# Kernel tuning notes

Hardware: AMD Instinct MI355X
Metric: run time of the kernel (lower is better)

The kernel has to match this reference:

```python
import jax, jax.numpy as jnp
import numpy as np

DN = ('NDHWC', 'DHWIO', 'NDHWC')
EPS = 1e-5  # torch BatchNorm default

def _conv(x, w, s):
    # Minkowski conv, kernel 3 centered: output coord j gathers input coords s*j + {-1,0,1}
    return jax.lax.conv_general_dilated(x, w, (s, s, s), ((1, 1),) * 3, dimension_numbers=DN)

def _convt(x, w):
    # stride-2 transpose conv, kernel 3 centered: output p gets input c where 2c in {p-1,p,p+1}
    return jax.lax.conv_general_dilated(x, w, (1, 1, 1), ((1, 2),) * 3,
                                        lhs_dilation=(2, 2, 2), dimension_numbers=DN)

def _down(m):
    # stride-2 coordinate map: a coarse voxel is active iff any of its 2x2x2 fine voxels is
    B, G = m.shape[0], m.shape[1]
    return m.reshape(B, G // 2, 2, G // 2, 2, G // 2, 2).any(axis=(2, 4, 6))

def _mbn(h, m, g, b):
    # MinkowskiBatchNorm: BatchNorm1d over the active (sparse) feature rows only
    mf = m[..., None].astype(h.dtype)
    h = h * mf
    cnt = jnp.maximum(jnp.sum(mf), 1.0)
    mean = jnp.sum(h, axis=(0, 1, 2, 3)) / cnt
    var = jnp.sum(((h - mean) * mf) ** 2, axis=(0, 1, 2, 3)) / cnt
    return ((h - mean) * jax.lax.rsqrt(var + EPS) * g + b) * mf


def setup_inputs() -> dict:
    key = jax.random.key(0)
    ks = jax.random.split(key, 8)
    B, G, Cin, Cout = 2, 64, 4, 16
    def w(k, shape, fan):
        return jax.random.normal(k, shape, jnp.float32) * np.float32(1.0 / np.sqrt(fan))
    return {
        'x': jax.random.normal(ks[0], (B, G, G, G, Cin), jnp.float32),
        'mask': jax.random.bernoulli(ks[1], 0.1, (B, G, G, G)),
        'w1': w(ks[2], (3, 3, 3, Cin, 8), 27 * Cin), 'g1': jnp.ones(8), 'b1': jnp.zeros(8),
        'w2': w(ks[3], (3, 3, 3, 8, 16), 27 * 8), 'g2': jnp.ones(16), 'b2': jnp.zeros(16),
        'w3': w(ks[4], (3, 3, 3, 16, 32), 27 * 16), 'g3': jnp.ones(32), 'b3': jnp.zeros(32),
        'w3t': w(ks[5], (3, 3, 3, 32, 16), 27 * 32), 'g3t': jnp.ones(16), 'b3t': jnp.zeros(16),
        'w2t': w(ks[6], (3, 3, 3, 32, 16), 27 * 32), 'g2t': jnp.ones(16), 'b2t': jnp.zeros(16),
        'w1x1': w(ks[7], (24, Cout), 24),
    }


def reference(x, mask, w1, g1, b1, w2, g2, b2, w3, g3, b3,
              w3t, g3t, b3t, w2t, g2t, b2t, w1x1):
    m1 = mask
    m2 = _down(m1)
    m4 = _down(m2)
    mf1 = m1[..., None].astype(x.dtype)

    xs = x * mf1                                      # sparse tensor: zero at inactive coords
    s1 = _mbn(_conv(xs, w1, 1), m1, g1, b1)           # block1, stride 1
    o = jax.nn.relu(s1)
    s2 = _mbn(_conv(o, w2, 2), m2, g2, b2)            # block2, stride 2
    o = jax.nn.relu(s2)
    s4 = _mbn(_conv(o, w3, 2), m4, g3, b3)            # block3, stride 4
    o = jax.nn.relu(s4)

    o = jax.nn.relu(_mbn(_convt(o, w3t), m2, g3t, b3t))   # block3_tr -> stride-2 coords
    o = jnp.concatenate([o, s2], axis=-1)                 # ME.cat(out, out_s2) -> 32 ch
    o = jax.nn.relu(_mbn(_convt(o, w2t), m1, g2t, b2t))   # block2_tr -> stride-1 coords
    o = jnp.concatenate([o, s1], axis=-1)                 # ME.cat(out, out_s1) -> 24 ch
    return jnp.einsum('bdhwc,co->bdhwo', o, w1x1) * mf1   # conv1_tr: 1x1x1 conv
```

## Files before the change

kernel.cpp:

```cpp
#include <hip/hip_runtime.h>

#define NVOX1 524288
#define NVOX2 65536
#define NVOX4 8192

#define ST_SUM1 16
#define ST_SQ1  24
#define ST_SUM2 32
#define ST_SQ2  48
#define ST_SUM3 64
#define ST_SQ3  96
#define ST_SUM3T 128
#define ST_SQ3T  144
#define ST_SUM2T 160
#define ST_SQ2T  176
#define FLAG_OFF 200
#define IC_N1 204
#define IC_N2 205
#define IC_N4 206
#define ST_ZERO 256

#define OFF_M1C 512
#define OFF_M2  (OFF_M1C + NVOX1)
#define OFF_M4  (OFF_M2 + NVOX2)
#define OFF_H1  (OFF_M4 + NVOX4)
#define OFF_S2  (OFF_H1 + NVOX1 * 8)
#define OFF_H3  (OFF_S2 + NVOX2 * 16)
#define OFF_T3  (OFF_H3 + NVOX4 * 32)
#define OFF_L1  (OFF_T3 + NVOX2 * 16)
#define OFF_L2  (OFF_L1 + NVOX1)
#define OFF_L4  (OFF_L2 + NVOX2)
#define OFF_BC1 (OFF_L4 + NVOX4)
#define OFF_BC2 (OFF_BC1 + 2048)
#define OFF_BC4 (OFF_BC2 + 256)

#define EPSBN 1e-5f

__device__ __forceinline__ void ttaps(int p, int gin, int* c, int* k, int* ok) {
  c[0] = p >> 1; k[0] = (p & 1) ? 0 : 1; ok[0] = 1;
  int cb = (p + 1) >> 1;
  int o = (p & 1) && (cb < gin);
  c[1] = o ? cb : 0; k[1] = 2; ok[1] = o;
}

__device__ __forceinline__ void stat_flush8(float* sum, float* sq, float* s_sum, float* s_sq, int t) {
#pragma unroll
  for (int off = 1; off < 64; off <<= 1)
#pragma unroll
    for (int c = 0; c < 8; c++) {
      sum[c] += __shfl_xor(sum[c], off, 64);
      sq[c]  += __shfl_xor(sq[c], off, 64);
    }
  if ((t & 63) == 0) {
#pragma unroll
    for (int c = 0; c < 8; c++) { atomicAdd(&s_sum[c], sum[c]); atomicAdd(&s_sq[c], sq[c]); }
  }
}

__global__ __launch_bounds__(256) void k_detect(const unsigned int* __restrict__ m,
                                                int* __restrict__ flags) {
  int tid = blockIdx.x * 256 + threadIdx.x;
  int hasf = 0, hasb = 0;
  for (int i = tid; i < NVOX1; i += 256 * 256) {
    unsigned int v = m[i];
    if (v == 0x3F800000u) hasf = 1;
    else if (v > 1u) hasb = 1;
  }
  hasf = __syncthreads_or(hasf);
  hasb = __syncthreads_or(hasb);
  if (threadIdx.x == 0) {
    if (hasf) atomicOr(&flags[0], 1);
    if (hasb) atomicOr(&flags[1], 1);
  }
}

__global__ __launch_bounds__(256) void k_canon(const void* __restrict__ mraw,
                                               int* __restrict__ m1c,
                                               const int* __restrict__ flags,
                                               int* __restrict__ blkcnt1) {
  int idx = blockIdx.x * 256 + threadIdx.x;
  int isf = flags[0], isb = flags[1];
  int v;
  if (isf)      v = (((const float*)mraw)[idx] != 0.f);
  else if (isb) v = (((const unsigned char*)mraw)[idx] != 0);
  else          v = (((const int*)mraw)[idx] != 0);
  m1c[idx] = v;
  int c = __syncthreads_count(v);
  if (threadIdx.x == 0) blkcnt1[blockIdx.x] = c;
}

__global__ __launch_bounds__(256) void k_down1(const int* __restrict__ m1,
                                               int* __restrict__ m2,
                                               int* __restrict__ blkcnt2) {
  int idx = blockIdx.x * 256 + threadIdx.x;
  int x = idx & 31, y = (idx >> 5) & 31, z = (idx >> 10) & 31, b = idx >> 15;
  int any = 0;
#pragma unroll
  for (int dz = 0; dz < 2; dz++)
#pragma unroll
    for (int dy = 0; dy < 2; dy++)
#pragma unroll
      for (int dx = 0; dx < 2; dx++)
        any |= m1[((b * 64 + 2 * z + dz) * 64 + 2 * y + dy) * 64 + 2 * x + dx];
  any = any ? 1 : 0;
  m2[idx] = any;
  int c = __syncthreads_count(any);
  if (threadIdx.x == 0) blkcnt2[blockIdx.x] = c;
}

__global__ __launch_bounds__(256) void k_down2(const int* __restrict__ m2,
                                               int* __restrict__ m4,
                                               int* __restrict__ blkcnt4) {
  int idx = blockIdx.x * 256 + threadIdx.x;
  int x = idx & 15, y = (idx >> 4) & 15, z = (idx >> 8) & 15, b = idx >> 12;
  int any = 0;
#pragma unroll
  for (int dz = 0; dz < 2; dz++)
#pragma unroll
    for (int dy = 0; dy < 2; dy++)
#pragma unroll
      for (int dx = 0; dx < 2; dx++)
        any |= m2[((b * 32 + 2 * z + dz) * 32 + 2 * y + dy) * 32 + 2 * x + dx];
  any = any ? 1 : 0;
  m4[idx] = any;
  int c = __syncthreads_count(any);
  if (threadIdx.x == 0) blkcnt4[blockIdx.x] = c;
}

__global__ __launch_bounds__(1024) void k_scan(int* __restrict__ bc1,
                                               int* __restrict__ bc2,
                                               int* __restrict__ bc4,
                                               int* __restrict__ cnts) {
  __shared__ int sA[2048], sB[2048];
  int* a; int n; int outIdx;
  if (blockIdx.x == 0)      { a = bc1; n = 2048; outIdx = IC_N1; }
  else if (blockIdx.x == 1) { a = bc2; n = 256;  outIdx = IC_N2; }
  else                      { a = bc4; n = 32;   outIdx = IC_N4; }
  int t = threadIdx.x;
  int i0 = t, i1 = t + 1024;
  int v0 = (i0 < n) ? a[i0] : 0;
  int v1 = (i1 < n) ? a[i1] : 0;
  sA[i0] = v0; sA[i1] = v1;
  __syncthreads();
  int* src = sA; int* dst = sB;
  for (int st = 1; st < 2048; st <<= 1) {
    int x0 = src[i0]; if (i0 >= st) x0 += src[i0 - st];
    int x1 = src[i1]; if (i1 >= st) x1 += src[i1 - st];
    dst[i0] = x0; dst[i1] = x1;
    __syncthreads();
    int* tmp = src; src = dst; dst = tmp;
  }
  if (i0 < n) a[i0] = src[i0] - v0;
  if (i1 < n) a[i1] = src[i1] - v1;
  if (t == 0) cnts[outIdx] = src[2047];
}

__global__ __launch_bounds__(256) void k_scatter(const int* __restrict__ m1,
                                                 const int* __restrict__ m2,
                                                 const int* __restrict__ m4,
                                                 const int* __restrict__ bc1,
                                                 const int* __restrict__ bc2,
                                                 const int* __restrict__ bc4,
                                                 int* __restrict__ list1,
                                                 int* __restrict__ list2,
                                                 int* __restrict__ list4) {
  __shared__ int s_w[4];
  int bid = blockIdx.x, t = threadIdx.x;
  const int* mask; const int* base; int* list; int lb;
  if (bid < 2048)      { mask = m1; base = bc1; list = list1; lb = bid; }
  else if (bid < 2304) { mask = m2; base = bc2; list = list2; lb = bid - 2048; }
  else                 { mask = m4; base = bc4; list = list4; lb = bid - 2304; }
  int idx = lb * 256 + t;
  int act = mask[idx];
  unsigned long long b = __ballot(act != 0);
  int lane = t & 63, wid = t >> 6;
  if (lane == 0) s_w[wid] = __popcll(b);
  __syncthreads();
  int wbase = 0;
  for (int i = 0; i < wid; i++) wbase += s_w[i];
  if (act) {
    int pre = __popcll(b & ((1ull << lane) - 1ull));
    list[base[lb] + wbase + pre] = idx;
  }
}

__global__ __launch_bounds__(256) void k_conv1(const float* __restrict__ x,
                                               const int* __restrict__ m1,
                                               const int* __restrict__ list1,
                                               const int* __restrict__ cnts,
                                               const float* __restrict__ w,
                                               float* __restrict__ h1,
                                               float* __restrict__ stats) {
  __shared__ float s_w[27 * 32];
  __shared__ float s_sum[8], s_sq[8];
  int t = threadIdx.x;
  { const float4* w4 = (const float4*)w; float4* sw4 = (float4*)s_w;
    for (int i = t; i < 216; i += 256) sw4[i] = w4[i]; }
  if (t < 8) { s_sum[t] = 0.f; s_sq[t] = 0.f; }
  __syncthreads();
  int n = cnts[IC_N1];
  float sum[8], sq[8];
#pragma unroll
  for (int c = 0; c < 8; c++) { sum[c] = 0.f; sq[c] = 0.f; }
  for (int i = blockIdx.x * 256 + t; i < n; i += gridDim.x * 256) {
    int v = list1[i];
    int vx = v & 63, vy = (v >> 6) & 63, vz = (v >> 12) & 63, vb = v >> 18;
    float acc[8];
#pragma unroll
    for (int c = 0; c < 8; c++) acc[c] = 0.f;
#pragma unroll
    for (int kd = 0; kd < 3; kd++) { int d = vz + kd - 1; if ((unsigned)d >= 64u) continue;
#pragma unroll
      for (int kh = 0; kh < 3; kh++) { int h = vy + kh - 1; if ((unsigned)h >= 64u) continue;
#pragma unroll
        for (int kw = 0; kw < 3; kw++) { int ww = vx + kw - 1; if ((unsigned)ww >= 64u) continue;
          int ni = ((vb * 64 + d) * 64 + h) * 64 + ww;
          if (!m1[ni]) continue;
          float4 ip = *(const float4*)(x + (size_t)ni * 4);
          const float* wp = s_w + ((kd * 3 + kh) * 3 + kw) * 32;
#pragma unroll
          for (int co = 0; co < 8; co++) {
            float a = fmaf(ip.x, wp[co], acc[co]);
            a = fmaf(ip.y, wp[8 + co], a);
            a = fmaf(ip.z, wp[16 + co], a);
            acc[co] = fmaf(ip.w, wp[24 + co], a);
          }
        } } }
    float4* hp = (float4*)(h1 + (size_t)v * 8);
    float4 q0 = {acc[0], acc[1], acc[2], acc[3]};
    float4 q1 = {acc[4], acc[5], acc[6], acc[7]};
    hp[0] = q0; hp[1] = q1;
#pragma unroll
    for (int c = 0; c < 8; c++) { sum[c] += acc[c]; sq[c] += acc[c] * acc[c]; }
  }
  stat_flush8(sum, sq, s_sum, s_sq, t);
  __syncthreads();
  if (t < 8) {
    if (s_sum[t] != 0.f) atomicAdd(&stats[ST_SUM1 + t], s_sum[t]);
    if (s_sq[t]  != 0.f) atomicAdd(&stats[ST_SQ1 + t], s_sq[t]);
  }
}

__global__ __launch_bounds__(256) void k_conv2(const float* __restrict__ h1,
                                               const int* __restrict__ m1,
                                               const int* __restrict__ list2,
                                               const int* __restrict__ cnts,
                                               const float* __restrict__ w,
                                               const float* __restrict__ g1,
                                               const float* __restrict__ b1,
                                               float* __restrict__ s2,
                                               float* __restrict__ stats) {
  __shared__ float s_w[27 * 8 * 8];
  __shared__ float s_sc[8], s_bi[8];
  __shared__ float s_sum[8], s_sq[8];
  int t = threadIdx.x, g = blockIdx.y;
  for (int i = t; i < 432; i += 256) {
    int r = i >> 1, half = i & 1;
    *(float4*)(s_w + r * 8 + half * 4) = *(const float4*)(w + r * 16 + g * 8 + half * 4);
  }
  if (t < 8) {
    float cnt = fmaxf((float)cnts[IC_N1], 1.f);
    float mean = stats[ST_SUM1 + t] / cnt;
    float var = fmaxf(stats[ST_SQ1 + t] / cnt - mean * mean, 0.f);
    float sc = g1[t] * rsqrtf(var + EPSBN);
    s_sc[t] = sc; s_bi[t] = b1[t] - mean * sc;
    s_sum[t] = 0.f; s_sq[t] = 0.f;
  }
  __syncthreads();
  int n = cnts[IC_N2];
  float sum[8], sq[8];
#pragma unroll
  for (int c = 0; c < 8; c++) { sum[c] = 0.f; sq[c] = 0.f; }
  for (int i = blockIdx.x * 256 + t; i < n; i += gridDim.x * 256) {
    int v = list2[i];
    int vx = v & 31, vy = (v >> 5) & 31, vz = (v >> 10) & 31, vb = v >> 15;
    float acc[8];
#pragma unroll
    for (int c = 0; c < 8; c++) acc[c] = 0.f;
#pragma unroll
    for (int kd = 0; kd < 3; kd++) { int d = 2 * vz + kd - 1; if (d < 0) continue;
#pragma unroll
      for (int kh = 0; kh < 3; kh++) { int h = 2 * vy + kh - 1; if (h < 0) continue;
#pragma unroll
        for (int kw = 0; kw < 3; kw++) { int ww = 2 * vx + kw - 1; if (ww < 0) continue;
          int ni = ((vb * 64 + d) * 64 + h) * 64 + ww;
          if (!m1[ni]) continue;
          float4 i0 = *(const float4*)(h1 + (size_t)ni * 8);
          float4 i1 = *(const float4*)(h1 + (size_t)ni * 8 + 4);
          float r[8] = {i0.x, i0.y, i0.z, i0.w, i1.x, i1.y, i1.z, i1.w};
          const float* wp = s_w + ((kd * 3 + kh) * 3 + kw) * 64;
#pragma unroll
          for (int ci = 0; ci < 8; ci++) {
            float vv = fmaxf(fmaf(r[ci], s_sc[ci], s_bi[ci]), 0.f);
#pragma unroll
            for (int co = 0; co < 8; co++) acc[co] = fmaf(vv, wp[ci * 8 + co], acc[co]);
          }
        } } }
    float4* sp = (float4*)(s2 + (size_t)v * 16 + g * 8);
    float4 q0 = {acc[0], acc[1], acc[2], acc[3]};
    float4 q1 = {acc[4], acc[5], acc[6], acc[7]};
    sp[0] = q0; sp[1] = q1;
#pragma unroll
    for (int c = 0; c < 8; c++) { sum[c] += acc[c]; sq[c] += acc[c] * acc[c]; }
  }
  stat_flush8(sum, sq, s_sum, s_sq, t);
  __syncthreads();
  if (t < 8) {
    if (s_sum[t] != 0.f) atomicAdd(&stats[ST_SUM2 + g * 8 + t], s_sum[t]);
    if (s_sq[t]  != 0.f) atomicAdd(&stats[ST_SQ2 + g * 8 + t], s_sq[t]);
  }
}

__global__ __launch_bounds__(256) void k_conv3(const float* __restrict__ s2raw,
                                               const int* __restrict__ m2,
                                               const int* __restrict__ list4,
                                               const int* __restrict__ cnts,
                                               const float* __restrict__ w,
                                               const float* __restrict__ g2,
                                               const float* __restrict__ b2,
                                               float* __restrict__ h3,
                                               float* __restrict__ stats) {
  __shared__ float s_w[27 * 16 * 8];
  __shared__ float s_sc[16], s_bi[16];
  __shared__ float s_sum[8], s_sq[8];
  int t = threadIdx.x, g = blockIdx.y;
  for (int i = t; i < 864; i += 256) {
    int r = i >> 1, half = i & 1;
    *(float4*)(s_w + r * 8 + half * 4) = *(const float4*)(w + r * 32 + g * 8 + half * 4);
  }
  if (t < 16) {
    float cnt = fmaxf((float)cnts[IC_N2], 1.f);
    float mean = stats[ST_SUM2 + t] / cnt;
    float var = fmaxf(stats[ST_SQ2 + t] / cnt - mean * mean, 0.f);
    float sc = g2[t] * rsqrtf(var + EPSBN);
    s_sc[t] = sc; s_bi[t] = b2[t] - mean * sc;
  }
  if (t < 8) { s_sum[t] = 0.f; s_sq[t] = 0.f; }
  __syncthreads();
  int n = cnts[IC_N4];
  float sum[8], sq[8];
#pragma unroll
  for (int c = 0; c < 8; c++) { sum[c] = 0.f; sq[c] = 0.f; }
  for (int i = blockIdx.x * 256 + t; i < n; i += gridDim.x * 256) {
    int v = list4[i];
    int vx = v & 15, vy = (v >> 4) & 15, vz = (v >> 8) & 15, vb = v >> 12;
    float acc[8];
#pragma unroll
    for (int c = 0; c < 8; c++) acc[c] = 0.f;
#pragma unroll
    for (int kd = 0; kd < 3; kd++) { int d = 2 * vz + kd - 1; if (d < 0) continue;
#pragma unroll
      for (int kh = 0; kh < 3; kh++) { int h = 2 * vy + kh - 1; if (h < 0) continue;
#pragma unroll
        for (int kw = 0; kw < 3; kw++) { int ww = 2 * vx + kw - 1; if (ww < 0) continue;
          int ni = ((vb * 32 + d) * 32 + h) * 32 + ww;
          if (!m2[ni]) continue;
          const float4* ip = (const float4*)(s2raw + (size_t)ni * 16);
          const float* wp = s_w + ((kd * 3 + kh) * 3 + kw) * 128;
#pragma unroll
          for (int cq = 0; cq < 4; cq++) {
            float4 q = ip[cq];
            float rr[4] = {q.x, q.y, q.z, q.w};
#pragma unroll
            for (int j = 0; j < 4; j++) {
              int ci = cq * 4 + j;
              float vv = fmaxf(fmaf(rr[j], s_sc[ci], s_bi[ci]), 0.f);
#pragma unroll
              for (int co = 0; co < 8; co++) acc[co] = fmaf(vv, wp[ci * 8 + co], acc[co]);
            }
          }
        } } }
    float4* hp = (float4*)(h3 + (size_t)v * 32 + g * 8);
    float4 q0 = {acc[0], acc[1], acc[2], acc[3]};
    float4 q1 = {acc[4], acc[5], acc[6], acc[7]};
    hp[0] = q0; hp[1] = q1;
#pragma unroll
    for (int c = 0; c < 8; c++) { sum[c] += acc[c]; sq[c] += acc[c] * acc[c]; }
  }
  stat_flush8(sum, sq, s_sum, s_sq, t);
  __syncthreads();
  if (t < 8) {
    if (s_sum[t] != 0.f) atomicAdd(&stats[ST_SUM3 + g * 8 + t], s_sum[t]);
    if (s_sq[t]  != 0.f) atomicAdd(&stats[ST_SQ3 + g * 8 + t], s_sq[t]);
  }
}

__global__ __launch_bounds__(256) void k_convt3(const float* __restrict__ h3raw,
                                                const int* __restrict__ m4,
                                                const int* __restrict__ list2,
                                                const int* __restrict__ cnts,
                                                const float* __restrict__ w,
                                                const float* __restrict__ g3,
                                                const float* __restrict__ b3,
                                                float* __restrict__ t3,
                                                float* __restrict__ stats) {
  __shared__ float s_w[27 * 32 * 8];
  __shared__ float s_sc[32], s_bi[32];
  __shared__ float s_sum[8], s_sq[8];
  int t = threadIdx.x, g = blockIdx.y;
  for (int i = t; i < 1728; i += 256) {
    int r = i >> 1, half = i & 1;
    *(float4*)(s_w + r * 8 + half * 4) = *(const float4*)(w + r * 16 + g * 8 + half * 4);
  }
  if (t < 32) {
    float cnt = fmaxf((float)cnts[IC_N4], 1.f);
    float mean = stats[ST_SUM3 + t] / cnt;
    float var = fmaxf(stats[ST_SQ3 + t] / cnt - mean * mean, 0.f);
    float sc = g3[t] * rsqrtf(var + EPSBN);
    s_sc[t] = sc; s_bi[t] = b3[t] - mean * sc;
  }
  if (t < 8) { s_sum[t] = 0.f; s_sq[t] = 0.f; }
  __syncthreads();
  int n = cnts[IC_N2];
  float sum[8], sq[8];
#pragma unroll
  for (int c = 0; c < 8; c++) { sum[c] = 0.f; sq[c] = 0.f; }
  for (int i = blockIdx.x * 256 + t; i < n; i += gridDim.x * 256) {
    int v = list2[i];
    int px = v & 31, py = (v >> 5) & 31, pz = (v >> 10) & 31, vb = v >> 15;
    int czv[2], kzv[2], okz[2], cyv[2], kyv[2], oky[2], cxv[2], kxv[2], okx[2];
    ttaps(pz, 16, czv, kzv, okz);
    ttaps(py, 16, cyv, kyv, oky);
    ttaps(px, 16, cxv, kxv, okx);
    float acc[8];
#pragma unroll
    for (int c = 0; c < 8; c++) acc[c] = 0.f;
#pragma unroll
    for (int dz = 0; dz < 2; dz++)
#pragma unroll
      for (int dy = 0; dy < 2; dy++)
#pragma unroll
        for (int dx = 0; dx < 2; dx++) {
          if (!(okz[dz] & oky[dy] & okx[dx])) continue;
          int ni = ((vb * 16 + czv[dz]) * 16 + cyv[dy]) * 16 + cxv[dx];
          if (!m4[ni]) continue;
          const float4* ip = (const float4*)(h3raw + (size_t)ni * 32);
          const float* wp = s_w + ((kzv[dz] * 3 + kyv[dy]) * 3 + kxv[dx]) * 256;
#pragma unroll
          for (int cq = 0; cq < 8; cq++) {
            float4 q = ip[cq];
            float rr[4] = {q.x, q.y, q.z, q.w};
#pragma unroll
            for (int j = 0; j < 4; j++) {
              int ci = cq * 4 + j;
              float vv = fmaxf(fmaf(rr[j], s_sc[ci], s_bi[ci]), 0.f);
#pragma unroll
              for (int co = 0; co < 8; co++) acc[co] = fmaf(vv, wp[ci * 8 + co], acc[co]);
            }
          }
        }
    float4* op = (float4*)(t3 + (size_t)v * 16 + g * 8);
    float4 q0 = {acc[0], acc[1], acc[2], acc[3]};
    float4 q1 = {acc[4], acc[5], acc[6], acc[7]};
    op[0] = q0; op[1] = q1;
#pragma unroll
    for (int c = 0; c < 8; c++) { sum[c] += acc[c]; sq[c] += acc[c] * acc[c]; }
  }
  stat_flush8(sum, sq, s_sum, s_sq, t);
  __syncthreads();
  if (t < 8) {
    if (s_sum[t] != 0.f) atomicAdd(&stats[ST_SUM3T + g * 8 + t], s_sum[t]);
    if (s_sq[t]  != 0.f) atomicAdd(&stats[ST_SQ3T + g * 8 + t], s_sq[t]);
  }
}

__global__ __launch_bounds__(256) void k_convt2(const float* __restrict__ t3raw,
                                                const float* __restrict__ s2raw,
                                                const int* __restrict__ m2,
                                                const int* __restrict__ list1,
                                                const int* __restrict__ cnts,
                                                const float* __restrict__ w,
                                                const float* __restrict__ g3t,
                                                const float* __restrict__ b3t,
                                                const float* __restrict__ g2,
                                                const float* __restrict__ b2,
                                                float* __restrict__ outraw,
                                                float* __restrict__ stats) {
  __shared__ float s_w[27 * 32 * 8];
  __shared__ float s_sct[16], s_bit[16], s_sc2[16], s_bi2[16];
  __shared__ float s_sum[8], s_sq[8];
  int t = threadIdx.x, g = blockIdx.y;
  for (int i = t; i < 1728; i += 256) {
    int r = i >> 1, half = i & 1;
    *(float4*)(s_w + r * 8 + half * 4) = *(const float4*)(w + r * 16 + g * 8 + half * 4);
  }
  if (t < 16) {
    float cnt = fmaxf((float)cnts[IC_N2], 1.f);
    float mean = stats[ST_SUM3T + t] / cnt;
    float var = fmaxf(stats[ST_SQ3T + t] / cnt - mean * mean, 0.f);
    float sc = g3t[t] * rsqrtf(var + EPSBN);
    s_sct[t] = sc; s_bit[t] = b3t[t] - mean * sc;
    float mean2 = stats[ST_SUM2 + t] / cnt;
    float var2 = fmaxf(stats[ST_SQ2 + t] / cnt - mean2 * mean2, 0.f);
    float sc2 = g2[t] * rsqrtf(var2 + EPSBN);
    s_sc2[t] = sc2; s_bi2[t] = b2[t] - mean2 * sc2;
  }
  if (t < 8) { s_sum[t] = 0.f; s_sq[t] = 0.f; }
  __syncthreads();
  int n = cnts[IC_N1];
  float sum[8], sq[8];
#pragma unroll
  for (int c = 0; c < 8; c++) { sum[c] = 0.f; sq[c] = 0.f; }
  for (int i = blockIdx.x * 256 + t; i < n; i += gridDim.x * 256) {
    int v = list1[i];
    int px = v & 63, py = (v >> 6) & 63, pz = (v >> 12) & 63, vb = v >> 18;
    int czv[2], kzv[2], okz[2], cyv[2], kyv[2], oky[2], cxv[2], kxv[2], okx[2];
    ttaps(pz, 32, czv, kzv, okz);
    ttaps(py, 32, cyv, kyv, oky);
    ttaps(px, 32, cxv, kxv, okx);
    float acc[8];
#pragma unroll
    for (int c = 0; c < 8; c++) acc[c] = 0.f;
#pragma unroll
    for (int dz = 0; dz < 2; dz++)
#pragma unroll
      for (int dy = 0; dy < 2; dy++)
#pragma unroll
        for (int dx = 0; dx < 2; dx++) {
          if (!(okz[dz] & oky[dy] & okx[dx])) continue;
          int ni = ((vb * 32 + czv[dz]) * 32 + cyv[dy]) * 32 + cxv[dx];
          if (!m2[ni]) continue;
          const float4* tp = (const float4*)(t3raw + (size_t)ni * 16);
          const float4* sp = (const float4*)(s2raw + (size_t)ni * 16);
          const float* wp = s_w + ((kzv[dz] * 3 + kyv[dy]) * 3 + kxv[dx]) * 256;
#pragma unroll
          for (int cq = 0; cq < 4; cq++) {
            float4 q = tp[cq];
            float rr[4] = {q.x, q.y, q.z, q.w};
#pragma unroll
            for (int j = 0; j < 4; j++) {
              int ci = cq * 4 + j;
              float vv = fmaxf(fmaf(rr[j], s_sct[ci], s_bit[ci]), 0.f);
#pragma unroll
              for (int co = 0; co < 8; co++) acc[co] = fmaf(vv, wp[ci * 8 + co], acc[co]);
            }
          }
#pragma unroll
          for (int cq = 0; cq < 4; cq++) {
            float4 q = sp[cq];
            float rr[4] = {q.x, q.y, q.z, q.w};
#pragma unroll
            for (int j = 0; j < 4; j++) {
              int ci = cq * 4 + j;
              float vv = fmaf(rr[j], s_sc2[ci], s_bi2[ci]);
#pragma unroll
              for (int co = 0; co < 8; co++) acc[co] = fmaf(vv, wp[(16 + ci) * 8 + co], acc[co]);
            }
          }
        }
    float4* op = (float4*)(outraw + (size_t)v * 16 + g * 8);
    float4 q0 = {acc[0], acc[1], acc[2], acc[3]};
    float4 q1 = {acc[4], acc[5], acc[6], acc[7]};
    op[0] = q0; op[1] = q1;
#pragma unroll
    for (int c = 0; c < 8; c++) { sum[c] += acc[c]; sq[c] += acc[c] * acc[c]; }
  }
  stat_flush8(sum, sq, s_sum, s_sq, t);
  __syncthreads();
  if (t < 8) {
    if (s_sum[t] != 0.f) atomicAdd(&stats[ST_SUM2T + g * 8 + t], s_sum[t]);
    if (s_sq[t]  != 0.f) atomicAdd(&stats[ST_SQ2T + g * 8 + t], s_sq[t]);
  }
}

__global__ __launch_bounds__(256) void k_final(float* __restrict__ out,
                                               const float* __restrict__ h1raw,
                                               const int* __restrict__ m1,
                                               const int* __restrict__ cnts,
                                               const float* __restrict__ g2t,
                                               const float* __restrict__ b2t,
                                               const float* __restrict__ g1,
                                               const float* __restrict__ b1,
                                               const float* __restrict__ w1x1,
                                               const float* __restrict__ stats) {
  __shared__ float s_sc[16], s_bi[16], s_sc1[8], s_bi1[8], s_w[384];
  int t = threadIdx.x;
  for (int i = t; i < 384; i += 256) s_w[i] = w1x1[i];
  if (t < 16) {
    float cnt = fmaxf((float)cnts[IC_N1], 1.f);
    float mean = stats[ST_SUM2T + t] / cnt;
    float var = fmaxf(stats[ST_SQ2T + t] / cnt - mean * mean, 0.f);
    float sc = g2t[t] * rsqrtf(var + EPSBN);
    s_sc[t] = sc; s_bi[t] = b2t[t] - mean * sc;
  }
  if (t < 8) {
    float cnt = fmaxf((float)cnts[IC_N1], 1.f);
    float mean = stats[ST_SUM1 + t] / cnt;
    float var = fmaxf(stats[ST_SQ1 + t] / cnt - mean * mean, 0.f);
    float sc = g1[t] * rsqrtf(var + EPSBN);
    s_sc1[t] = sc; s_bi1[t] = b1[t] - mean * sc;
  }
  __syncthreads();
  int v = blockIdx.x * 256 + t;
  float* op = out + (size_t)v * 16;
  float4* op4 = (float4*)op;
  if (!m1[v]) {
    float4 z = {0.f, 0.f, 0.f, 0.f};
    op4[0] = z; op4[1] = z; op4[2] = z; op4[3] = z;
    return;
  }
  float t2[16];
  {
#pragma unroll
    for (int cq = 0; cq < 4; cq++) {
      float4 q = op4[cq];
      t2[cq * 4 + 0] = fmaxf(fmaf(q.x, s_sc[cq * 4 + 0], s_bi[cq * 4 + 0]), 0.f);
      t2[cq * 4 + 1] = fmaxf(fmaf(q.y, s_sc[cq * 4 + 1], s_bi[cq * 4 + 1]), 0.f);
      t2[cq * 4 + 2] = fmaxf(fmaf(q.z, s_sc[cq * 4 + 2], s_bi[cq * 4 + 2]), 0.f);
      t2[cq * 4 + 3] = fmaxf(fmaf(q.w, s_sc[cq * 4 + 3], s_bi[cq * 4 + 3]), 0.f);
    }
  }
  float s1v[8];
  {
    const float4* sp4 = (const float4*)(h1raw + (size_t)v * 8);
#pragma unroll
    for (int cq = 0; cq < 2; cq++) {
      float4 q = sp4[cq];
      s1v[cq * 4 + 0] = fmaf(q.x, s_sc1[cq * 4 + 0], s_bi1[cq * 4 + 0]);
      s1v[cq * 4 + 1] = fmaf(q.y, s_sc1[cq * 4 + 1], s_bi1[cq * 4 + 1]);
      s1v[cq * 4 + 2] = fmaf(q.z, s_sc1[cq * 4 + 2], s_bi1[cq * 4 + 2]);
      s1v[cq * 4 + 3] = fmaf(q.w, s_sc1[cq * 4 + 3], s_bi1[cq * 4 + 3]);
    }
  }
  float o[16];
#pragma unroll
  for (int oc = 0; oc < 16; oc++) o[oc] = 0.f;
#pragma unroll
  for (int c = 0; c < 16; c++) {
    float vv = t2[c];
#pragma unroll
    for (int oc = 0; oc < 16; oc++) o[oc] = fmaf(vv, s_w[c * 16 + oc], o[oc]);
  }
#pragma unroll
  for (int c = 0; c < 8; c++) {
    float vv = s1v[c];
#pragma unroll
    for (int oc = 0; oc < 16; oc++) o[oc] = fmaf(vv, s_w[(16 + c) * 16 + oc], o[oc]);
  }
#pragma unroll
  for (int cq = 0; cq < 4; cq++) {
    float4 q = {o[cq * 4 + 0], o[cq * 4 + 1], o[cq * 4 + 2], o[cq * 4 + 3]};
    op4[cq] = q;
  }
}

extern "C" void kernel_launch(void* const* d_in, const int* in_sizes, int n_in,
                              void* d_out, int out_size, void* d_ws, size_t ws_size,
                              hipStream_t stream) {
  const float* x    = (const float*)d_in[0];
  const void*  mraw = d_in[1];
  const float* w1   = (const float*)d_in[2];
  const float* g1   = (const float*)d_in[3];
  const float* b1   = (const float*)d_in[4];
  const float* w2   = (const float*)d_in[5];
  const float* g2   = (const float*)d_in[6];
  const float* b2   = (const float*)d_in[7];
  const float* w3   = (const float*)d_in[8];
  const float* g3   = (const float*)d_in[9];
  const float* b3   = (const float*)d_in[10];
  const float* w3t  = (const float*)d_in[11];
  const float* g3t  = (const float*)d_in[12];
  const float* b3t  = (const float*)d_in[13];
  const float* w2t  = (const float*)d_in[14];
  const float* g2t  = (const float*)d_in[15];
  const float* b2t  = (const float*)d_in[16];
  const float* w1x1 = (const float*)d_in[17];

  float* ws = (float*)d_ws;
  float* stats = ws;
  int* cnts = (int*)ws;
  int* flags = (int*)(ws + FLAG_OFF);
  int* m1c = (int*)(ws + OFF_M1C);
  int* m2  = (int*)(ws + OFF_M2);
  int* m4  = (int*)(ws + OFF_M4);
  float* h1 = ws + OFF_H1;
  float* s2 = ws + OFF_S2;
  float* h3 = ws + OFF_H3;
  float* t3 = ws + OFF_T3;
  int* list1 = (int*)(ws + OFF_L1);
  int* list2 = (int*)(ws + OFF_L2);
  int* list4 = (int*)(ws + OFF_L4);
  int* bc1 = (int*)(ws + OFF_BC1);
  int* bc2 = (int*)(ws + OFF_BC2);
  int* bc4 = (int*)(ws + OFF_BC4);
  float* out = (float*)d_out;

  hipMemsetAsync(ws, 0, ST_ZERO * sizeof(float), stream);
  k_detect<<<256, 256, 0, stream>>>((const unsigned int*)mraw, flags);
  k_canon<<<NVOX1 / 256, 256, 0, stream>>>(mraw, m1c, flags, bc1);
  k_down1<<<NVOX2 / 256, 256, 0, stream>>>(m1c, m2, bc2);
  k_down2<<<NVOX4 / 256, 256, 0, stream>>>(m2, m4, bc4);
  k_scan<<<3, 1024, 0, stream>>>(bc1, bc2, bc4, cnts);
  k_scatter<<<2048 + 256 + 32, 256, 0, stream>>>(m1c, m2, m4, bc1, bc2, bc4, list1, list2, list4);
  k_conv1<<<256, 256, 0, stream>>>(x, m1c, list1, cnts, w1, h1, stats);
  k_conv2<<<dim3(256, 2), 256, 0, stream>>>(h1, m1c, list2, cnts, w2, g1, b1, s2, stats);
  k_conv3<<<dim3(32, 4), 256, 0, stream>>>(s2, m2, list4, cnts, w3, g2, b2, h3, stats);
  k_convt3<<<dim3(256, 2), 256, 0, stream>>>(h3, m4, list2, cnts, w3t, g3, b3, t3, stats);
  k_convt2<<<dim3(256, 2), 256, 0, stream>>>(t3, s2, m2, list1, cnts, w2t, g3t, b3t, g2, b2, out, stats);
  k_final<<<NVOX1 / 256, 256, 0, stream>>>(out, h1, m1c, cnts, g2t, b2t, g1, b1, w1x1, stats);
}
```

Measured before the change: 201.5 us.

## Precompute per-voxel neighbor bitmasks in one kernel shared by all convolutions

Adds a k_nbr kernel that, for each active voxel at each level, builds a bitmask of which kernel taps hit active input voxels (27 taps for the convs, 8 combinations for the transposed convs). The conv kernels then read one int per voxel and test bits, rather than doing scattered mask loads and bounds checks inline. The mask gathers are not removed; they move into a separate pass. That pass costs an extra launch, extra memory traffic and workspace, and the conv2 gathers are wasted when the second channel group recomputes nothing. The goal is to shorten the dependent load chains inside the heavy conv loops and make per-tap branching cheaper.

```diff
diff --git a/kernel.cpp b/kernel.cpp
--- a/kernel.cpp
+++ b/kernel.cpp
@@ -33,6 +33,11 @@
 #define OFF_BC1 (OFF_L4 + NVOX4)
 #define OFF_BC2 (OFF_BC1 + 2048)
 #define OFF_BC4 (OFF_BC2 + 256)
+#define OFF_NB1  (OFF_BC4 + 32)
+#define OFF_NB2  (OFF_NB1 + NVOX1)
+#define OFF_NB4  (OFF_NB2 + NVOX2)
+#define OFF_NBT3 (OFF_NB4 + NVOX4)
+#define OFF_NBT2 (OFF_NBT3 + NVOX2)
 
 #define EPSBN 1e-5f
 
@@ -184,8 +189,124 @@
   }
 }
 
+__global__ __launch_bounds__(256) void k_nbr(const int* __restrict__ m1,
+                                             const int* __restrict__ m2,
+                                             const int* __restrict__ m4,
+                                             const int* __restrict__ list1,
+                                             const int* __restrict__ list2,
+                                             const int* __restrict__ list4,
+                                             const int* __restrict__ cnts,
+                                             int* __restrict__ nb1,
+                                             int* __restrict__ nb2,
+                                             int* __restrict__ nb4,
+                                             int* __restrict__ nbt3,
+                                             int* __restrict__ nbt2) {
+  int mode = blockIdx.y;
+  int tid = blockIdx.x * 256 + threadIdx.x;
+  int stride = gridDim.x * 256;
+  if (mode == 0) {
+    int n = cnts[IC_N1];
+    for (int i = tid; i < n; i += stride) {
+      int v = list1[i];
+      int vx = v & 63, vy = (v >> 6) & 63, vz = (v >> 12) & 63, vb = v >> 18;
+      unsigned wbits = 0; int tap = 0;
+#pragma unroll
+      for (int kd = 0; kd < 3; kd++) { int d = vz + kd - 1; int okd = ((unsigned)d < 64u); int dc = okd ? d : 0;
+#pragma unroll
+        for (int kh = 0; kh < 3; kh++) { int h = vy + kh - 1; int okh = ((unsigned)h < 64u); int hc = okh ? h : 0;
+#pragma unroll
+          for (int kw = 0; kw < 3; kw++) { int ww = vx + kw - 1; int okw = ((unsigned)ww < 64u); int wc = okw ? ww : 0;
+            int ni = ((vb * 64 + dc) * 64 + hc) * 64 + wc;
+            int bit = (okd & okh & okw) & (m1[ni] != 0);
+            wbits |= ((unsigned)bit) << tap; tap++;
+          } } }
+      nb1[i] = (int)wbits;
+    }
+  } else if (mode == 1) {
+    int n = cnts[IC_N2];
+    for (int i = tid; i < n; i += stride) {
+      int v = list2[i];
+      int vx = v & 31, vy = (v >> 5) & 31, vz = (v >> 10) & 31, vb = v >> 15;
+      unsigned wbits = 0; int tap = 0;
+#pragma unroll
+      for (int kd = 0; kd < 3; kd++) { int d = 2 * vz + kd - 1; int okd = (d >= 0); int dc = okd ? d : 0;
+#pragma unroll
+        for (int kh = 0; kh < 3; kh++) { int h = 2 * vy + kh - 1; int okh = (h >= 0); int hc = okh ? h : 0;
+#pragma unroll
+          for (int kw = 0; kw < 3; kw++) { int ww = 2 * vx + kw - 1; int okw = (ww >= 0); int wc = okw ? ww : 0;
+            int ni = ((vb * 64 + dc) * 64 + hc) * 64 + wc;
+            int bit = (okd & okh & okw) & (m1[ni] != 0);
+            wbits |= ((unsigned)bit) << tap; tap++;
+          } } }
+      nb2[i] = (int)wbits;
+    }
+  } else if (mode == 2) {
+    int n = cnts[IC_N4];
+    for (int i = tid; i < n; i += stride) {
+      int v = list4[i];
+      int vx = v & 15, vy = (v >> 4) & 15, vz = (v >> 8) & 15, vb = v >> 12;
+      unsigned wbits = 0; int tap = 0;
+#pragma unroll
+      for (int kd = 0; kd < 3; kd++) { int d = 2 * vz + kd - 1; int okd = (d >= 0); int dc = okd ? d : 0;
+#pragma unroll
+        for (int kh = 0; kh < 3; kh++) { int h = 2 * vy + kh - 1; int okh = (h >= 0); int hc = okh ? h : 0;
+#pragma unroll
+          for (int kw = 0; kw < 3; kw++) { int ww = 2 * vx + kw - 1; int okw = (ww >= 0); int wc = okw ? ww : 0;
+            int ni = ((vb * 32 + dc) * 32 + hc) * 32 + wc;
+            int bit = (okd & okh & okw) & (m2[ni] != 0);
+            wbits |= ((unsigned)bit) << tap; tap++;
+          } } }
+      nb4[i] = (int)wbits;
+    }
+  } else if (mode == 3) {
+    int n = cnts[IC_N2];
+    for (int i = tid; i < n; i += stride) {
+      int v = list2[i];
+      int px = v & 31, py = (v >> 5) & 31, pz = (v >> 10) & 31, vb = v >> 15;
+      int czv[2], kzv[2], okz[2], cyv[2], kyv[2], oky[2], cxv[2], kxv[2], okx[2];
+      ttaps(pz, 16, czv, kzv, okz);
+      ttaps(py, 16, cyv, kyv, oky);
+      ttaps(px, 16, cxv, kxv, okx);
+      unsigned wbits = 0; int comb = 0;
+#pragma unroll
+      for (int dz = 0; dz < 2; dz++)
+#pragma unroll
+        for (int dy = 0; dy < 2; dy++)
+#pragma unroll
+          for (int dx = 0; dx < 2; dx++) {
+            int ni = ((vb * 16 + czv[dz]) * 16 + cyv[dy]) * 16 + cxv[dx];
+            int bit = (okz[dz] & oky[dy] & okx[dx]) & (m4[ni] != 0);
+            wbits |= ((unsigned)bit) << comb; comb++;
+          }
+      nbt3[i] = (int)wbits;
+    }
+  } else {
+    int n = cnts[IC_N1];
+    for (int i = tid; i < n; i += stride) {
+      int v = list1[i];
+      int px = v & 63, py = (v >> 6) & 63, pz = (v >> 12) & 63, vb = v >> 18;
+      int czv[2], kzv[2], okz[2], cyv[2], kyv[2], oky[2], cxv[2], kxv[2], okx[2];
+      ttaps(pz, 32, czv, kzv, okz);
+      ttaps(py, 32, cyv, kyv, oky);
+      ttaps(px, 32, cxv, kxv, okx);
+      unsigned wbits = 0; int comb = 0;
+#pragma unroll
+      for (int dz = 0; dz < 2; dz++)
+#pragma unroll
+        for (int dy = 0; dy < 2; dy++)
+#pragma unroll
+          for (int dx = 0; dx < 2; dx++) {
+            int ni = ((vb * 32 + czv[dz]) * 32 + cyv[dy]) * 32 + cxv[dx];
+            int bit = (okz[dz] & oky[dy] & okx[dx]) & (m2[ni] != 0);
+            wbits |= ((unsigned)bit) << comb; comb++;
+          }
+      nbt2[i] = (int)wbits;
+    }
+  }
+}
+
 __global__ __launch_bounds__(256) void k_conv1(const float* __restrict__ x,
-                                               const int* __restrict__ m1,
+                                               const int* __restrict__ nb1,
                                                const int* __restrict__ list1,
                                                const int* __restrict__ cnts,
                                                const float* __restrict__ w,
@@ -204,32 +325,35 @@
   for (int c = 0; c < 8; c++) { sum[c] = 0.f; sq[c] = 0.f; }
   for (int i = blockIdx.x * 256 + t; i < n; i += gridDim.x * 256) {
     int v = list1[i];
+    unsigned nbr = (unsigned)nb1[i];
     int vx = v & 63, vy = (v >> 6) & 63, vz = (v >> 12) & 63, vb = v >> 18;
     float acc[8];
 #pragma unroll
     for (int c = 0; c < 8; c++) acc[c] = 0.f;
-#pragma unroll
-    for (int kd = 0; kd < 3; kd++) { int d = vz + kd - 1; if ((unsigned)d >= 64u) continue;
-#pragma unroll
-      for (int kh = 0; kh < 3; kh++) { int h = vy + kh - 1; if ((unsigned)h >= 64u) continue;
-#pragma unroll
-        for (int kw = 0; kw < 3; kw++) { int ww = vx + kw - 1; if ((unsigned)ww >= 64u) continue;
-          int ni = ((vb * 64 + d) * 64 + h) * 64 + ww;
-          if (!m1[ni]) continue;
-          float4 ip = *(const float4*)(x + (size_t)ni * 4);
-          const float* wp = s_w + ((kd * 3 + kh) * 3 + kw) * 32;
-#pragma unroll
-          for (int co = 0; co < 8; co++) {
-            float a = fmaf(ip.x, wp[co], acc[co]);
-            a = fmaf(ip.y, wp[8 + co], a);
-            a = fmaf(ip.z, wp[16 + co], a);
-            acc[co] = fmaf(ip.w, wp[24 + co], a);
+    int tap = 0;
+#pragma unroll
+    for (int kd = 0; kd < 3; kd++)
+#pragma unroll
+      for (int kh = 0; kh < 3; kh++)
+#pragma unroll
+        for (int kw = 0; kw < 3; kw++) {
+          if (nbr & (1u << tap)) {
+            int ni = ((vb * 64 + vz + kd - 1) * 64 + vy + kh - 1) * 64 + vx + kw - 1;
+            float4 ip = *(const float4*)(x + (size_t)ni * 4);
+            const float* wp = s_w + tap * 32;
+#pragma unroll
+            for (int co = 0; co < 8; co++) {
+              float a = fmaf(ip.x, wp[co], acc[co]);
+              a = fmaf(ip.y, wp[8 + co], a);
+              a = fmaf(ip.z, wp[16 + co], a);
+              acc[co] = fmaf(ip.w, wp[24 + co], a);
+            }
           }
-        } } }
+          tap++;
+        }
     float4* hp = (float4*)(h1 + (size_t)v * 8);
-    float4 q0 = {acc[0], acc[1], acc[2], acc[3]};
-    float4 q1 = {acc[4], acc[5], acc[6], acc[7]};
-    hp[0] = q0; hp[1] = q1;
+    hp[0] = make_float4(acc[0], acc[1], acc[2], acc[3]);
+    hp[1] = make_float4(acc[4], acc[5], acc[6], acc[7]);
 #pragma unroll
     for (int c = 0; c < 8; c++) { sum[c] += acc[c]; sq[c] += acc[c] * acc[c]; }
   }
@@ -242,7 +366,7 @@
 }
 
 __global__ __launch_bounds__(256) void k_conv2(const float* __restrict__ h1,
-                                               const int* __restrict__ m1,
+                                               const int* __restrict__ nb2,
                                                const int* __restrict__ list2,
                                                const int* __restrict__ cnts,
                                                const float* __restrict__ w,
@@ -273,33 +397,36 @@
   for (int c = 0; c < 8; c++) { sum[c] = 0.f; sq[c] = 0.f; }
   for (int i = blockIdx.x * 256 + t; i < n; i += gridDim.x * 256) {
     int v = list2[i];
+    unsigned nbr = (unsigned)nb2[i];
     int vx = v & 31, vy = (v >> 5) & 31, vz = (v >> 10) & 31, vb = v >> 15;
     float acc[8];
 #pragma unroll
     for (int c = 0; c < 8; c++) acc[c] = 0.f;
-#pragma unroll
-    for (int kd = 0; kd < 3; kd++) { int d = 2 * vz + kd - 1; if (d < 0) continue;
-#pragma unroll
-      for (int kh = 0; kh < 3; kh++) { int h = 2 * vy + kh - 1; if (h < 0) continue;
-#pragma unroll
-        for (int kw = 0; kw < 3; kw++) { int ww = 2 * vx + kw - 1; if (ww < 0) continue;
-          int ni = ((vb * 64 + d) * 64 + h) * 64 + ww;
-          if (!m1[ni]) continue;
-          float4 i0 = *(const float4*)(h1 + (size_t)ni * 8);
-          float4 i1 = *(const float4*)(h1 + (size_t)ni * 8 + 4);
-          float r[8] = {i0.x, i0.y, i0.z, i0.w, i1.x, i1.y, i1.z, i1.w};
-          const float* wp = s_w + ((kd * 3 + kh) * 3 + kw) * 64;
-#pragma unroll
-          for (int ci = 0; ci < 8; ci++) {
-            float vv = fmaxf(fmaf(r[ci], s_sc[ci], s_bi[ci]), 0.f);
-#pragma unroll
-            for (int co = 0; co < 8; co++) acc[co] = fmaf(vv, wp[ci * 8 + co], acc[co]);
+    int tap = 0;
+#pragma unroll
+    for (int kd = 0; kd < 3; kd++)
+#pragma unroll
+      for (int kh = 0; kh < 3; kh++)
+#pragma unroll
+        for (int kw = 0; kw < 3; kw++) {
+          if (nbr & (1u << tap)) {
+            int ni = ((vb * 64 + 2 * vz + kd - 1) * 64 + 2 * vy + kh - 1) * 64 + 2 * vx + kw - 1;
+            float4 i0 = *(const float4*)(h1 + (size_t)ni * 8);
+            float4 i1 = *(const float4*)(h1 + (size_t)ni * 8 + 4);
+            float r[8] = {i0.x, i0.y, i0.z, i0.w, i1.x, i1.y, i1.z, i1.w};
+            const float* wp = s_w + tap * 64;
+#pragma unroll
+            for (int ci = 0; ci < 8; ci++) {
+              float vv = fmaxf(fmaf(r[ci], s_sc[ci], s_bi[ci]), 0.f);
+#pragma unroll
+              for (int co = 0; co < 8; co++) acc[co] = fmaf(vv, wp[ci * 8 + co], acc[co]);
+            }
           }
-        } } }
+          tap++;
+        }
     float4* sp = (float4*)(s2 + (size_t)v * 16 + g * 8);
-    float4 q0 = {acc[0], acc[1], acc[2], acc[3]};
-    float4 q1 = {acc[4], acc[5], acc[6], acc[7]};
-    sp[0] = q0; sp[1] = q1;
+    sp[0] = make_float4(acc[0], acc[1], acc[2], acc[3]);
+    sp[1] = make_float4(acc[4], acc[5], acc[6], acc[7]);
 #pragma unroll
     for (int c = 0; c < 8; c++) { sum[c] += acc[c]; sq[c] += acc[c] * acc[c]; }
   }
@@ -312,7 +439,7 @@
 }
 
 __global__ __launch_bounds__(256) void k_conv3(const float* __restrict__ s2raw,
-                                               const int* __restrict__ m2,
+                                               const int* __restrict__ nb4,
                                                const int* __restrict__ list4,
                                                const int* __restrict__ cnts,
                                                const float* __restrict__ w,
@@ -343,37 +470,40 @@
   for (int c = 0; c < 8; c++) { sum[c] = 0.f; sq[c] = 0.f; }
   for (int i = blockIdx.x * 256 + t; i < n; i += gridDim.x * 256) {
     int v = list4[i];
+    unsigned nbr = (unsigned)nb4[i];
     int vx = v & 15, vy = (v >> 4) & 15, vz = (v >> 8) & 15, vb = v >> 12;
     float acc[8];
 #pragma unroll
     for (int c = 0; c < 8; c++) acc[c] = 0.f;
-#pragma unroll
-    for (int kd = 0; kd < 3; kd++) { int d = 2 * vz + kd - 1; if (d < 0) continue;
-#pragma unroll
-      for (int kh = 0; kh < 3; kh++) { int h = 2 * vy + kh - 1; if (h < 0) continue;
-#pragma unroll
-        for (int kw = 0; kw < 3; kw++) { int ww = 2 * vx + kw - 1; if (ww < 0) continue;
-          int ni = ((vb * 32 + d) * 32 + h) * 32 + ww;
-          if (!m2[ni]) continue;
-          const float4* ip = (const float4*)(s2raw + (size_t)ni * 16);
-          const float* wp = s_w + ((kd * 3 + kh) * 3 + kw) * 128;
-#pragma unroll
-          for (int cq = 0; cq < 4; cq++) {
-            float4 q = ip[cq];
-            float rr[4] = {q.x, q.y, q.z, q.w};
-#pragma unroll
-            for (int j = 0; j < 4; j++) {
-              int ci = cq * 4 + j;
-              float vv = fmaxf(fmaf(rr[j], s_sc[ci], s_bi[ci]), 0.f);
-#pragma unroll
-              for (int co = 0; co < 8; co++) acc[co] = fmaf(vv, wp[ci * 8 + co], acc[co]);
+    int tap = 0;
+#pragma unroll
+    for (int kd = 0; kd < 3; kd++)
+#pragma unroll
+      for (int kh = 0; kh < 3; kh++)
+#pragma unroll
+        for (int kw = 0; kw < 3; kw++) {
+          if (nbr & (1u << tap)) {
+            int ni = ((vb * 32 + 2 * vz + kd - 1) * 32 + 2 * vy + kh - 1) * 32 + 2 * vx + kw - 1;
+            const float4* ip = (const float4*)(s2raw + (size_t)ni * 16);
+            const float* wp = s_w + tap * 128;
+#pragma unroll
+            for (int cq = 0; cq < 4; cq++) {
+              float4 q = ip[cq];
+              float rr[4] = {q.x, q.y, q.z, q.w};
+#pragma unroll
+              for (int j = 0; j < 4; j++) {
+                int ci = cq * 4 + j;
+                float vv = fmaxf(fmaf(rr[j], s_sc[ci], s_bi[ci]), 0.f);
+#pragma unroll
+                for (int co = 0; co < 8; co++) acc[co] = fmaf(vv, wp[ci * 8 + co], acc[co]);
+              }
             }
           }
-        } } }
+          tap++;
+        }
     float4* hp = (float4*)(h3 + (size_t)v * 32 + g * 8);
-    float4 q0 = {acc[0], acc[1], acc[2], acc[3]};
-    float4 q1 = {acc[4], acc[5], acc[6], acc[7]};
-    hp[0] = q0; hp[1] = q1;
+    hp[0] = make_float4(acc[0], acc[1], acc[2], acc[3]);
+    hp[1] = make_float4(acc[4], acc[5], acc[6], acc[7]);
 #pragma unroll
     for (int c = 0; c < 8; c++) { sum[c] += acc[c]; sq[c] += acc[c] * acc[c]; }
   }
@@ -386,7 +516,7 @@
 }
 
 __global__ __launch_bounds__(256) void k_convt3(const float* __restrict__ h3raw,
-                                                const int* __restrict__ m4,
+                                                const int* __restrict__ nbt3,
                                                 const int* __restrict__ list2,
                                                 const int* __restrict__ cnts,
                                                 const float* __restrict__ w,
@@ -417,6 +547,7 @@
   for (int c = 0; c < 8; c++) { sum[c] = 0.f; sq[c] = 0.f; }
   for (int i = blockIdx.x * 256 + t; i < n; i += gridDim.x * 256) {
     int v = list2[i];
+    unsigned nbr = (unsigned)nbt3[i];
     int px = v & 31, py = (v >> 5) & 31, pz = (v >> 10) & 31, vb = v >> 15;
     int czv[2], kzv[2], okz[2], cyv[2], kyv[2], oky[2], cxv[2], kxv[2], okx[2];
     ttaps(pz, 16, czv, kzv, okz);
@@ -425,34 +556,35 @@
     float acc[8];
 #pragma unroll
     for (int c = 0; c < 8; c++) acc[c] = 0.f;
+    int comb = 0;
 #pragma unroll
     for (int dz = 0; dz < 2; dz++)
 #pragma unroll
       for (int dy = 0; dy < 2; dy++)
 #pragma unroll
         for (int dx = 0; dx < 2; dx++) {
-          if (!(okz[dz] & oky[dy] & okx[dx])) continue;
-          int ni = ((vb * 16 + czv[dz]) * 16 + cyv[dy]) * 16 + cxv[dx];
-          if (!m4[ni]) continue;
-          const float4* ip = (const float4*)(h3raw + (size_t)ni * 32);
-          const float* wp = s_w + ((kzv[dz] * 3 + kyv[dy]) * 3 + kxv[dx]) * 256;
-#pragma unroll
-          for (int cq = 0; cq < 8; cq++) {
-            float4 q = ip[cq];
-            float rr[4] = {q.x, q.y, q.z, q.w};
-#pragma unroll
-            for (int j = 0; j < 4; j++) {
-              int ci = cq * 4 + j;
-              float vv = fmaxf(fmaf(rr[j], s_sc[ci], s_bi[ci]), 0.f);
-#pragma unroll
-              for (int co = 0; co < 8; co++) acc[co] = fmaf(vv, wp[ci * 8 + co], acc[co]);
+          if (nbr & (1u << comb)) {
+            int ni = ((vb * 16 + czv[dz]) * 16 + cyv[dy]) * 16 + cxv[dx];
+            const float4* ip = (const float4*)(h3raw + (size_t)ni * 32);
+            const float* wp = s_w + ((kzv[dz] * 3 + kyv[dy]) * 3 + kxv[dx]) * 256;
+#pragma unroll
+            for (int cq = 0; cq < 8; cq++) {
+              float4 q = ip[cq];
+              float rr[4] = {q.x, q.y, q.z, q.w};
+#pragma unroll
+              for (int j = 0; j < 4; j++) {
+                int ci = cq * 4 + j;
+                float vv = fmaxf(fmaf(rr[j], s_sc[ci], s_bi[ci]), 0.f);
+#pragma unroll
+                for (int co = 0; co < 8; co++) acc[co] = fmaf(vv, wp[ci * 8 + co], acc[co]);
+              }
             }
           }
+          comb++;
         }
     float4* op = (float4*)(t3 + (size_t)v * 16 + g * 8);
-    float4 q0 = {acc[0], acc[1], acc[2], acc[3]};
-    float4 q1 = {acc[4], acc[5], acc[6], acc[7]};
-    op[0] = q0; op[1] = q1;
+    op[0] = make_float4(acc[0], acc[1], acc[2], acc[3]);
+    op[1] = make_float4(acc[4], acc[5], acc[6], acc[7]);
 #pragma unroll
     for (int c = 0; c < 8; c++) { sum[c] += acc[c]; sq[c] += acc[c] * acc[c]; }
   }
@@ -466,7 +598,7 @@
 
 __global__ __launch_bounds__(256) void k_convt2(const float* __restrict__ t3raw,
                                                 const float* __restrict__ s2raw,
-                                                const int* __restrict__ m2,
+                                                const int* __restrict__ nbt2,
                                                 const int* __restrict__ list1,
                                                 const int* __restrict__ cnts,
                                                 const float* __restrict__ w,
@@ -503,6 +635,7 @@
   for (int c = 0; c < 8; c++) { sum[c] = 0.f; sq[c] = 0.f; }
   for (int i = blockIdx.x * 256 + t; i < n; i += gridDim.x * 256) {
     int v = list1[i];
+    unsigned nbr = (unsigned)nbt2[i];
     int px = v & 63, py = (v >> 6) & 63, pz = (v >> 12) & 63, vb = v >> 18;
     int czv[2], kzv[2], okz[2], cyv[2], kyv[2], oky[2], cxv[2], kxv[2], okx[2];
     ttaps(pz, 32, czv, kzv, okz);
@@ -511,47 +644,48 @@
     float acc[8];
 #pragma unroll
     for (int c = 0; c < 8; c++) acc[c] = 0.f;
+    int comb = 0;
 #pragma unroll
     for (int dz = 0; dz < 2; dz++)
 #pragma unroll
       for (int dy = 0; dy < 2; dy++)
 #pragma unroll
         for (int dx = 0; dx < 2; dx++) {
-          if (!(okz[dz] & oky[dy] & okx[dx])) continue;
-          int ni = ((vb * 32 + czv[dz]) * 32 + cyv[dy]) * 32 + cxv[dx];
-          if (!m2[ni]) continue;
-          const float4* tp = (const float4*)(t3raw + (size_t)ni * 16);
-          const float4* sp = (const float4*)(s2raw + (size_t)ni * 16);
-          const float* wp = s_w + ((kzv[dz] * 3 + kyv[dy]) * 3 + kxv[dx]) * 256;
-#pragma unroll
-          for (int cq = 0; cq < 4; cq++) {
-            float4 q = tp[cq];
-            float rr[4] = {q.x, q.y, q.z, q.w};
-#pragma unroll
-            for (int j = 0; j < 4; j++) {
-              int ci = cq * 4 + j;
-              float vv = fmaxf(fmaf(rr[j], s_sct[ci], s_bit[ci]), 0.f);
-#pragma unroll
-              for (int co = 0; co < 8; co++) acc[co] = fmaf(vv, wp[ci * 8 + co], acc[co]);
+          if (nbr & (1u << comb)) {
+            int ni = ((vb * 32 + czv[dz]) * 32 + cyv[dy]) * 32 + cxv[dx];
+            const float4* tp = (const float4*)(t3raw + (size_t)ni * 16);
+            const float4* sp = (const float4*)(s2raw + (size_t)ni * 16);
+            const float* wp = s_w + ((kzv[dz] * 3 + kyv[dy]) * 3 + kxv[dx]) * 256;
+#pragma unroll
+            for (int cq = 0; cq < 4; cq++) {
+              float4 q = tp[cq];
+              float rr[4] = {q.x, q.y, q.z, q.w};
+#pragma unroll
+              for (int j = 0; j < 4; j++) {
+                int ci = cq * 4 + j;
+                float vv = fmaxf(fmaf(rr[j], s_sct[ci], s_bit[ci]), 0.f);
+#pragma unroll
+                for (int co = 0; co < 8; co++) acc[co] = fmaf(vv, wp[ci * 8 + co], acc[co]);
+              }
+            }
+#pragma unroll
+            for (int cq = 0; cq < 4; cq++) {
+              float4 q = sp[cq];
+              float rr[4] = {q.x, q.y, q.z, q.w};
+#pragma unroll
+              for (int j = 0; j < 4; j++) {
+                int ci = cq * 4 + j;
+                float vv = fmaf(rr[j], s_sc2[ci], s_bi2[ci]);
+#pragma unroll
+                for (int co = 0; co < 8; co++) acc[co] = fmaf(vv, wp[(16 + ci) * 8 + co], acc[co]);
+              }
             }
           }
-#pragma unroll
-          for (int cq = 0; cq < 4; cq++) {
-            float4 q = sp[cq];
-            float rr[4] = {q.x, q.y, q.z, q.w};
-#pragma unroll
-            for (int j = 0; j < 4; j++) {
-              int ci = cq * 4 + j;
-              float vv = fmaf(rr[j], s_sc2[ci], s_bi2[ci]);
-#pragma unroll
-              for (int co = 0; co < 8; co++) acc[co] = fmaf(vv, wp[(16 + ci) * 8 + co], acc[co]);
-            }
-          }
+          comb++;
         }
     float4* op = (float4*)(outraw + (size_t)v * 16 + g * 8);
-    float4 q0 = {acc[0], acc[1], acc[2], acc[3]};
-    float4 q1 = {acc[4], acc[5], acc[6], acc[7]};
-    op[0] = q0; op[1] = q1;
+    op[0] = make_float4(acc[0], acc[1], acc[2], acc[3]);
+    op[1] = make_float4(acc[4], acc[5], acc[6], acc[7]);
 #pragma unroll
     for (int c = 0; c < 8; c++) { sum[c] += acc[c]; sq[c] += acc[c] * acc[c]; }
   }
@@ -683,6 +817,11 @@
   int* bc1 = (int*)(ws + OFF_BC1);
   int* bc2 = (int*)(ws + OFF_BC2);
   int* bc4 = (int*)(ws + OFF_BC4);
+  int* nb1  = (int*)(ws + OFF_NB1);
+  int* nb2  = (int*)(ws + OFF_NB2);
+  int* nb4  = (int*)(ws + OFF_NB4);
+  int* nbt3 = (int*)(ws + OFF_NBT3);
+  int* nbt2 = (int*)(ws + OFF_NBT2);
   float* out = (float*)d_out;
 
   hipMemsetAsync(ws, 0, ST_ZERO * sizeof(float), stream);
@@ -692,10 +831,12 @@
   k_down2<<<NVOX4 / 256, 256, 0, stream>>>(m2, m4, bc4);
   k_scan<<<3, 1024, 0, stream>>>(bc1, bc2, bc4, cnts);
   k_scatter<<<2048 + 256 + 32, 256, 0, stream>>>(m1c, m2, m4, bc1, bc2, bc4, list1, list2, list4);
-  k_conv1<<<256, 256, 0, stream>>>(x, m1c, list1, cnts, w1, h1, stats);
-  k_conv2<<<dim3(256, 2), 256, 0, stream>>>(h1, m1c, list2, cnts, w2, g1, b1, s2, stats);
-  k_conv3<<<dim3(32, 4), 256, 0, stream>>>(s2, m2, list4, cnts, w3, g2, b2, h3, stats);
-  k_convt3<<<dim3(256, 2), 256, 0, stream>>>(h3, m4, list2, cnts, w3t, g3, b3, t3, stats);
-  k_convt2<<<dim3(256, 2), 256, 0, stream>>>(t3, s2, m2, list1, cnts, w2t, g3t, b3t, g2, b2, out, stats);
+  k_nbr<<<dim3(256, 5), 256, 0, stream>>>(m1c, m2, m4, list1, list2, list4, cnts,
+                                          nb1, nb2, nb4, nbt3, nbt2);
+  k_conv1<<<256, 256, 0, stream>>>(x, nb1, list1, cnts, w1, h1, stats);
+  k_conv2<<<dim3(256, 2), 256, 0, stream>>>(h1, nb2, list2, cnts, w2, g1, b1, s2, stats);
+  k_conv3<<<dim3(32, 4), 256, 0, stream>>>(s2, nb4, list4, cnts, w3, g2, b2, h3, stats);
+  k_convt3<<<dim3(256, 2), 256, 0, stream>>>(h3, nbt3, list2, cnts, w3t, g3, b3, t3, stats);
+  k_convt2<<<dim3(256, 2), 256, 0, stream>>>(t3, s2, nbt2, list1, cnts, w2t, g3t, b3t, g2, b2, out, stats);
   k_final<<<NVOX1 / 256, 256, 0, stream>>>(out, h1, m1c, cnts, g2t, b2t, g1, b1, w1x1, stats);
 }
```

Measured after the change: 191.4 us. 1.05x faster.
